# Kernel optimization log

Hardware: AMD Instinct MI355X
Metric: run time of the kernel (lower is better)

The kernel has to match this reference:

```python
import jax, jax.numpy as jnp
import numpy as np

N = 50000          # number of parent nodes / neighborhoods
D_IN = 256         # input_size
K = 8              # points decoded per neighborhood
GLOBAL_DIMS = [256, 128, 64]
FC_DIMS = [256, 256, 256]


def _linear_params(key, d_in, d_out):
    kw, kb = jax.random.split(key)
    W = jax.random.normal(kw, (d_in, d_out), dtype=jnp.float32) * 0.05
    b = jax.random.normal(kb, (d_out,), dtype=jnp.float32) * 0.05
    return W, b


def setup_inputs() -> dict:
    key = jax.random.key(0)
    keys = jax.random.split(key, 8)
    inp = {"input_features": jax.random.normal(keys[0], (N, D_IN), dtype=jnp.float32)}
    # global MLP: 256 -> 256 -> 128 -> 64
    d = D_IN
    for i, nb in enumerate(GLOBAL_DIMS):
        W, b = _linear_params(keys[1 + i], d, nb)
        inp[f"Wg{i}"], inp[f"bg{i}"] = W, b
        d = nb
    # neighborhood decoder head: 64 -> K*3
    inp["Wdec"], inp["bdec"] = _linear_params(keys[4], GLOBAL_DIMS[-1], K * 3)
    # per-point MLP: (256 + 64 + 3) -> 256 -> 256 -> 256
    d = D_IN + GLOBAL_DIMS[-1] + 3
    for i, nb in enumerate(FC_DIMS):
        W, b = _linear_params(keys[5 + i], d, nb)
        inp[f"W{i}"], inp[f"b{i}"] = W, b
        d = nb
    return inp


def reference(input_features, Wg0, bg0, Wg1, bg1, Wg2, bg2, Wdec, bdec,
              W0, b0, W1, b1, W2, b2):
    relu = jax.nn.relu
    # global feature MLP on node features: [N, 256] -> [N, 64]
    feats = input_features
    for W, b in ((Wg0, bg0), (Wg1, bg1), (Wg2, bg2)):
        feats = relu(feats @ W + b)
    # neighborhood decoder: K relative 3D points per node -> [N*K, 3]
    relative_points = (feats @ Wdec + bdec).reshape(-1, 3)
    cluster = jnp.repeat(jnp.arange(N, dtype=jnp.int32), K)  # [N*K]
    # gather (duplicate) parent features per decoded point
    nbr_dup = jnp.take(feats, cluster, axis=0)               # [N*K, 64]
    inp_dup = jnp.take(input_features, cluster, axis=0)      # [N*K, 256]
    decoded = jnp.concatenate([inp_dup, nbr_dup, relative_points], axis=1)  # [N*K, 323]
    for W, b in ((W0, b0), (W1, b1), (W2, b2)):
        decoded = relu(decoded @ W + b)
    return relative_points, decoded, cluster
```

## Files before the change

kernel.cpp:

```cpp
#include <hip/hip_runtime.h>
#include <hip/hip_bf16.h>

typedef __attribute__((ext_vector_type(8))) __bf16 bf16x8;
typedef __attribute__((ext_vector_type(4))) float f32x4;

#define NN 50000
#define TM1 16
#define NODES2 8


__device__ __forceinline__ unsigned short f2bf(float f) {
    unsigned int u = __builtin_bit_cast(unsigned int, f);
    u = (u + 0x7FFFu + ((u >> 16) & 1u)) >> 16;
    return (unsigned short)u;
}

__global__ __launch_bounds__(256) void k_prep(
    const float* __restrict__ W0, const float* __restrict__ W1,
    const float* __restrict__ W2, unsigned short* __restrict__ wbf)
{
    int idx = blockIdx.x * 256 + threadIdx.x;
    if (idx < 81920) {
        int n = idx / 320, k = idx - n * 320;
        wbf[idx] = f2bf(W0[(size_t)k * 256 + n]);
    } else if (idx < 147456) {
        int e = idx - 81920;
        int n = e >> 8, k = e & 255;
        wbf[idx] = f2bf(W1[(size_t)k * 256 + n]);
    } else if (idx < 212992) {
        int e = idx - 147456;
        int n = e >> 8, k = e & 255;
        wbf[idx] = f2bf(W2[(size_t)k * 256 + n]);
    }
}

__global__ __launch_bounds__(256) void k_global(
    const float* __restrict__ x,
    const float* __restrict__ Wg0, const float* __restrict__ bg0,
    const float* __restrict__ Wg1, const float* __restrict__ bg1,
    const float* __restrict__ Wg2, const float* __restrict__ bg2,
    const float* __restrict__ Wdec, const float* __restrict__ bdec,
    float* __restrict__ feats_ws,
    float* __restrict__ out_rel,
    float* __restrict__ out_cluster)
{
    __shared__ __attribute__((aligned(16))) float xin[TM1 * 256];
    __shared__ __attribute__((aligned(16))) float h0[TM1 * 256];
    __shared__ __attribute__((aligned(16))) float g1[TM1 * 128];
    __shared__ __attribute__((aligned(16))) float g2[TM1 * 64];

    const int tid = threadIdx.x;
    const int blk = blockIdx.x;

    {
        const float4* xg = (const float4*)(x + (size_t)blk * TM1 * 256);
        float4* xl = (float4*)xin;
        #pragma unroll
        for (int it = 0; it < 4; ++it) xl[tid + it * 256] = xg[tid + it * 256];
    }
    __syncthreads();

    {
        const int j = tid;
        float acc[TM1];
        float b = bg0[j];
        #pragma unroll
        for (int m = 0; m < TM1; ++m) acc[m] = b;
        for (int i = 0; i < 256; i += 4) {
            float w0 = Wg0[(size_t)(i + 0) * 256 + j];
            float w1 = Wg0[(size_t)(i + 1) * 256 + j];
            float w2 = Wg0[(size_t)(i + 2) * 256 + j];
            float w3 = Wg0[(size_t)(i + 3) * 256 + j];
            #pragma unroll
            for (int m = 0; m < TM1; ++m) {
                float4 xv = *(const float4*)&xin[m * 256 + i];
                acc[m] += xv.x * w0 + xv.y * w1 + xv.z * w2 + xv.w * w3;
            }
        }
        #pragma unroll
        for (int m = 0; m < TM1; ++m) h0[m * 256 + j] = fmaxf(acc[m], 0.f);
    }
    __syncthreads();

    {
        const int col = tid & 127;
        const int rg  = tid >> 7;
        float acc[8];
        float b = bg1[col];
        #pragma unroll
        for (int m = 0; m < 8; ++m) acc[m] = b;
        for (int i = 0; i < 256; i += 4) {
            float w0 = Wg1[(size_t)(i + 0) * 128 + col];
            float w1 = Wg1[(size_t)(i + 1) * 128 + col];
            float w2 = Wg1[(size_t)(i + 2) * 128 + col];
            float w3 = Wg1[(size_t)(i + 3) * 128 + col];
            #pragma unroll
            for (int m = 0; m < 8; ++m) {
                int r = rg * 8 + m;
                float4 xv = *(const float4*)&h0[r * 256 + i];
                acc[m] += xv.x * w0 + xv.y * w1 + xv.z * w2 + xv.w * w3;
            }
        }
        #pragma unroll
        for (int m = 0; m < 8; ++m) g1[(rg * 8 + m) * 128 + col] = fmaxf(acc[m], 0.f);
    }
    __syncthreads();

    {
        const int col = tid & 63;
        const int rg  = tid >> 6;
        float acc[4];
        float b = bg2[col];
        #pragma unroll
        for (int m = 0; m < 4; ++m) acc[m] = b;
        for (int i = 0; i < 128; i += 4) {
            float w0 = Wg2[(size_t)(i + 0) * 64 + col];
            float w1 = Wg2[(size_t)(i + 1) * 64 + col];
            float w2 = Wg2[(size_t)(i + 2) * 64 + col];
            float w3 = Wg2[(size_t)(i + 3) * 64 + col];
            #pragma unroll
            for (int m = 0; m < 4; ++m) {
                int r = rg * 4 + m;
                float4 xv = *(const float4*)&g1[r * 128 + i];
                acc[m] += xv.x * w0 + xv.y * w1 + xv.z * w2 + xv.w * w3;
            }
        }
        #pragma unroll
        for (int m = 0; m < 4; ++m) g2[(rg * 4 + m) * 64 + col] = fmaxf(acc[m], 0.f);
    }
    __syncthreads();

    {
        float4* fw = (float4*)(feats_ws + (size_t)blk * TM1 * 64);
        fw[tid] = ((const float4*)g2)[tid];
    }

    for (int tt = tid; tt < TM1 * 24; tt += 256) {
        int m = tt / 24;
        int c = tt - m * 24;
        float acc = bdec[c];
        for (int i = 0; i < 64; ++i) acc += g2[m * 64 + i] * Wdec[i * 24 + c];
        out_rel[(size_t)blk * (TM1 * 24) + tt] = acc;
    }

    if (tid < TM1 * 8) {
        out_cluster[(size_t)blk * (TM1 * 8) + tid] = (float)(blk * TM1 + (tid >> 3));
    }
}

__global__ __launch_bounds__(256) void k_points(
    const float* __restrict__ x,
    const float* __restrict__ feats_ws,
    const float* __restrict__ rel_in,
    const unsigned short* __restrict__ wbf,
    const float* __restrict__ W0f,
    const float* __restrict__ b0,
    const float* __restrict__ b1,
    const float* __restrict__ b2,
    float* __restrict__ out_dec)
{
    __shared__ __attribute__((aligned(16))) unsigned short h0s[64 * 264];
    __shared__ __attribute__((aligned(16))) unsigned short h1s[64 * 264];
    __shared__ __attribute__((aligned(16))) unsigned short xcat[NODES2 * 336];
    __shared__ __attribute__((aligned(16))) float w3buf[3 * 256];
    __shared__ __attribute__((aligned(16))) float rl[NODES2 * 24];
    float* s = (float*)h1s;

    const int tid  = threadIdx.x;
    const int lane = tid & 63;
    const int w    = tid >> 6;
    const int quad = lane >> 4;
    const int l15  = lane & 15;
    const int blk  = blockIdx.x;
    const size_t nb = (size_t)blk * NODES2;

    for (int e = tid; e < NODES2 * 256; e += 256) {
        int r = e >> 8, c = e & 255;
        xcat[r * 336 + c] = f2bf(x[(nb + r) * 256 + c]);
    }
    for (int e = tid; e < NODES2 * 64; e += 256) {
        int r = e >> 6, c = e & 63;
        xcat[r * 336 + 256 + c] = f2bf(feats_ws[(nb + r) * 64 + c]);
    }
    for (int e = tid; e < 3 * 256; e += 256) {
        int r = e >> 8, c = e & 255;
        w3buf[e] = W0f[(size_t)(320 + r) * 256 + c];
    }
    if (tid < NODES2 * 24) rl[tid] = rel_in[nb * 24 + tid];
    __syncthreads();

    {
        const unsigned short* W0t = wbf;
        f32x4 acc[4];
        f32x4 z = {0.f, 0.f, 0.f, 0.f};
        #pragma unroll
        for (int t = 0; t < 4; ++t) acc[t] = z;
        const unsigned short* arow = &xcat[(lane & 7) * 336];
        for (int ks = 0; ks < 10; ++ks) {
            int k0 = ks * 32 + quad * 8;
            bf16x8 a = *(const bf16x8*)(arow + k0);
            #pragma unroll
            for (int t = 0; t < 4; ++t) {
                int n = w * 64 + t * 16 + l15;
                bf16x8 b = *(const bf16x8*)(W0t + (size_t)n * 320 + k0);
                acc[t] = __builtin_amdgcn_mfma_f32_16x16x32_bf16(a, b, acc[t], 0, 0, 0);
            }
        }
        #pragma unroll
        for (int t = 0; t < 4; ++t) {
            int col = w * 64 + t * 16 + l15;
            float bb = b0[col];
            #pragma unroll
            for (int r = 0; r < 4; ++r) {
                int row = quad * 4 + r;
                if (row < NODES2) s[row * 256 + col] = acc[t][r] + bb;
            }
        }
    }
    __syncthreads();

    for (int it = 0; it < 16; ++it) {
        int task = tid + it * 256;
        int row = task >> 6;
        int cg  = task & 63;
        int node = row >> 3, p = row & 7;
        float4 sv = *(const float4*)&s[node * 256 + cg * 4];
        float ra = rl[node * 24 + p * 3 + 0];
        float rb = rl[node * 24 + p * 3 + 1];
        float rc = rl[node * 24 + p * 3 + 2];
        float4 wa = *(const float4*)&w3buf[cg * 4];
        float4 wbv = *(const float4*)&w3buf[256 + cg * 4];
        float4 wc = *(const float4*)&w3buf[512 + cg * 4];
        float v0 = fmaxf(sv.x + ra * wa.x + rb * wbv.x + rc * wc.x, 0.f);
        float v1 = fmaxf(sv.y + ra * wa.y + rb * wbv.y + rc * wc.y, 0.f);
        float v2 = fmaxf(sv.z + ra * wa.z + rb * wbv.z + rc * wc.z, 0.f);
        float v3 = fmaxf(sv.w + ra * wa.w + rb * wbv.w + rc * wc.w, 0.f);
        unsigned int lo = (unsigned int)f2bf(v0) | ((unsigned int)f2bf(v1) << 16);
        unsigned int hi = (unsigned int)f2bf(v2) | ((unsigned int)f2bf(v3) << 16);
        uint2 pk; pk.x = lo; pk.y = hi;
        *(uint2*)&h0s[row * 264 + cg * 4] = pk;
    }
    __syncthreads();

    {
        const unsigned short* W1t = wbf + 81920;
        f32x4 acc[4][4];
        f32x4 z = {0.f, 0.f, 0.f, 0.f};
        #pragma unroll
        for (int m = 0; m < 4; ++m)
            #pragma unroll
            for (int t = 0; t < 4; ++t) acc[m][t] = z;
        for (int ks = 0; ks < 8; ++ks) {
            int k0 = ks * 32 + quad * 8;
            bf16x8 a[4], b[4];
            #pragma unroll
            for (int m = 0; m < 4; ++m)
                a[m] = *(const bf16x8*)&h0s[(m * 16 + l15) * 264 + k0];
            #pragma unroll
            for (int t = 0; t < 4; ++t)
                b[t] = *(const bf16x8*)(W1t + (size_t)(w * 64 + t * 16 + l15) * 256 + k0);
            #pragma unroll
            for (int m = 0; m < 4; ++m)
                #pragma unroll
                for (int t = 0; t < 4; ++t)
                    acc[m][t] = __builtin_amdgcn_mfma_f32_16x16x32_bf16(a[m], b[t], acc[m][t], 0, 0, 0);
        }
        #pragma unroll
        for (int t = 0; t < 4; ++t) {
            int col = w * 64 + t * 16 + l15;
            float bb = b1[col];
            #pragma unroll
            for (int m = 0; m < 4; ++m) {
                #pragma unroll
                for (int r = 0; r < 4; ++r) {
                    int row = m * 16 + quad * 4 + r;
                    h1s[row * 264 + col] = f2bf(fmaxf(acc[m][t][r] + bb, 0.f));
                }
            }
        }
    }
    __syncthreads();

    {
        const unsigned short* W2t = wbf + 147456;
        f32x4 acc[4][4];
        f32x4 z = {0.f, 0.f, 0.f, 0.f};
        #pragma unroll
        for (int m = 0; m < 4; ++m)
            #pragma unroll
            for (int t = 0; t < 4; ++t) acc[m][t] = z;
        for (int ks = 0; ks < 8; ++ks) {
            int k0 = ks * 32 + quad * 8;
            bf16x8 a[4], b[4];
            #pragma unroll
            for (int m = 0; m < 4; ++m)
                a[m] = *(const bf16x8*)&h1s[(m * 16 + l15) * 264 + k0];
            #pragma unroll
            for (int t = 0; t < 4; ++t)
                b[t] = *(const bf16x8*)(W2t + (size_t)(w * 64 + t * 16 + l15) * 256 + k0);
            #pragma unroll
            for (int m = 0; m < 4; ++m)
                #pragma unroll
                for (int t = 0; t < 4; ++t)
                    acc[m][t] = __builtin_amdgcn_mfma_f32_16x16x32_bf16(a[m], b[t], acc[m][t], 0, 0, 0);
        }
        #pragma unroll
        for (int t = 0; t < 4; ++t) {
            int col = w * 64 + t * 16 + l15;
            float bb = b2[col];
            #pragma unroll
            for (int m = 0; m < 4; ++m) {
                #pragma unroll
                for (int r = 0; r < 4; ++r) {
                    int row = m * 16 + quad * 4 + r;
                    out_dec[(nb * 8 + row) * 256 + col] = fmaxf(acc[m][t][r] + bb, 0.f);
                }
            }
        }
    }
}

extern "C" void kernel_launch(void* const* d_in, const int* in_sizes, int n_in,
                              void* d_out, int out_size, void* d_ws, size_t ws_size,
                              hipStream_t stream) {
    const float* x    = (const float*)d_in[0];
    const float* Wg0  = (const float*)d_in[1];
    const float* bg0  = (const float*)d_in[2];
    const float* Wg1  = (const float*)d_in[3];
    const float* bg1  = (const float*)d_in[4];
    const float* Wg2  = (const float*)d_in[5];
    const float* bg2  = (const float*)d_in[6];
    const float* Wdec = (const float*)d_in[7];
    const float* bdec = (const float*)d_in[8];
    const float* W0   = (const float*)d_in[9];
    const float* b0   = (const float*)d_in[10];
    const float* W1   = (const float*)d_in[11];
    const float* b1   = (const float*)d_in[12];
    const float* W2   = (const float*)d_in[13];
    const float* b2   = (const float*)d_in[14];

    float* out      = (float*)d_out;
    float* out_rel  = out;
    float* out_dec  = out + 1200000;
    float* out_clu  = out + 103600000;

    unsigned short* wbf = (unsigned short*)d_ws;
    float* feats_ws = (float*)((char*)d_ws + 425984);

    k_prep<<<832, 256, 0, stream>>>(W0, W1, W2, wbf);
    k_global<<<NN / TM1, 256, 0, stream>>>(x, Wg0, bg0, Wg1, bg1, Wg2, bg2,
                                           Wdec, bdec, feats_ws, out_rel, out_clu);
    k_points<<<NN / NODES2, 256, 0, stream>>>(x, feats_ws, out_rel,
                                              wbf, W0, b0, b1, b2, out_dec);
}
```

Measured before the change: 1.059 ms.

## Run global MLP on MFMA with split-bf16 hi/lo emulation of fp32

The global 3-layer MLP moves from scalar fp32 FMA loops onto bf16 MFMA instructions. Activations and weights are split into high and low bf16 parts, using three MFMAs per step to keep close to fp32 accuracy. Weight transposition and splitting are added to the prep kernel. Node features are now stored as bf16, which halves that traffic and lets k_points copy them directly without converting. The costs are three times the MFMA work, extra LDS buffers, and a small precision change in the stored features.

```diff
diff --git a/kernel.cpp b/kernel.cpp
--- a/kernel.cpp
+++ b/kernel.cpp
@@ -3,21 +3,31 @@
 
 typedef __attribute__((ext_vector_type(8))) __bf16 bf16x8;
 typedef __attribute__((ext_vector_type(4))) float f32x4;
+typedef __attribute__((ext_vector_type(4))) unsigned short u16x4;
 
 #define NN 50000
 #define TM1 16
 #define NODES2 8
 
+
+#define FEATS_OFF 212992
+#define GW_OFF    3412992
 
 __device__ __forceinline__ unsigned short f2bf(float f) {
     unsigned int u = __builtin_bit_cast(unsigned int, f);
     u = (u + 0x7FFFu + ((u >> 16) & 1u)) >> 16;
     return (unsigned short)u;
 }
+__device__ __forceinline__ float bf2f(unsigned short h) {
+    return __builtin_bit_cast(float, (unsigned int)h << 16);
+}
 
 __global__ __launch_bounds__(256) void k_prep(
     const float* __restrict__ W0, const float* __restrict__ W1,
-    const float* __restrict__ W2, unsigned short* __restrict__ wbf)
+    const float* __restrict__ W2,
+    const float* __restrict__ Wg0, const float* __restrict__ Wg1,
+    const float* __restrict__ Wg2,
+    unsigned short* __restrict__ wbf)
 {
     int idx = blockIdx.x * 256 + threadIdx.x;
     if (idx < 81920) {
@@ -31,108 +41,168 @@
         int e = idx - 147456;
         int n = e >> 8, k = e & 255;
         wbf[idx] = f2bf(W2[(size_t)k * 256 + n]);
+    } else if (idx < 319488) {
+        int e = idx - 212992;
+        float v; int oh, ol;
+        if (e < 65536) {
+            int n = e >> 8, k = e & 255;
+            v = Wg0[(size_t)k * 256 + n];
+            oh = GW_OFF + e; ol = GW_OFF + 65536 + e;
+        } else if (e < 98304) {
+            int e2 = e - 65536;
+            int n = e2 >> 8, k = e2 & 255;
+            v = Wg1[(size_t)k * 128 + n];
+            oh = GW_OFF + 131072 + e2; ol = GW_OFF + 163840 + e2;
+        } else {
+            int e3 = e - 98304;
+            int n = e3 >> 7, k = e3 & 127;
+            v = Wg2[(size_t)k * 64 + n];
+            oh = GW_OFF + 196608 + e3; ol = GW_OFF + 204800 + e3;
+        }
+        unsigned short h = f2bf(v);
+        wbf[oh] = h;
+        wbf[ol] = f2bf(v - bf2f(h));
     }
 }
 
 __global__ __launch_bounds__(256) void k_global(
     const float* __restrict__ x,
-    const float* __restrict__ Wg0, const float* __restrict__ bg0,
-    const float* __restrict__ Wg1, const float* __restrict__ bg1,
-    const float* __restrict__ Wg2, const float* __restrict__ bg2,
+    const float* __restrict__ bg0, const float* __restrict__ bg1,
+    const float* __restrict__ bg2,
     const float* __restrict__ Wdec, const float* __restrict__ bdec,
-    float* __restrict__ feats_ws,
+    const unsigned short* __restrict__ gw,
+    unsigned short* __restrict__ feats_bf,
     float* __restrict__ out_rel,
     float* __restrict__ out_cluster)
 {
-    __shared__ __attribute__((aligned(16))) float xin[TM1 * 256];
-    __shared__ __attribute__((aligned(16))) float h0[TM1 * 256];
-    __shared__ __attribute__((aligned(16))) float g1[TM1 * 128];
+    __shared__ __attribute__((aligned(16))) unsigned short xh[TM1 * 264];
+    __shared__ __attribute__((aligned(16))) unsigned short xl[TM1 * 264];
+    __shared__ __attribute__((aligned(16))) unsigned short hh[TM1 * 264];
+    __shared__ __attribute__((aligned(16))) unsigned short hl[TM1 * 264];
+    __shared__ __attribute__((aligned(16))) unsigned short q1h[TM1 * 136];
+    __shared__ __attribute__((aligned(16))) unsigned short q1l[TM1 * 136];
     __shared__ __attribute__((aligned(16))) float g2[TM1 * 64];
 
-    const int tid = threadIdx.x;
-    const int blk = blockIdx.x;
-
-    {
-        const float4* xg = (const float4*)(x + (size_t)blk * TM1 * 256);
-        float4* xl = (float4*)xin;
-        #pragma unroll
-        for (int it = 0; it < 4; ++it) xl[tid + it * 256] = xg[tid + it * 256];
-    }
-    __syncthreads();
-
-    {
-        const int j = tid;
-        float acc[TM1];
-        float b = bg0[j];
-        #pragma unroll
-        for (int m = 0; m < TM1; ++m) acc[m] = b;
-        for (int i = 0; i < 256; i += 4) {
-            float w0 = Wg0[(size_t)(i + 0) * 256 + j];
-            float w1 = Wg0[(size_t)(i + 1) * 256 + j];
-            float w2 = Wg0[(size_t)(i + 2) * 256 + j];
-            float w3 = Wg0[(size_t)(i + 3) * 256 + j];
-            #pragma unroll
-            for (int m = 0; m < TM1; ++m) {
-                float4 xv = *(const float4*)&xin[m * 256 + i];
-                acc[m] += xv.x * w0 + xv.y * w1 + xv.z * w2 + xv.w * w3;
-            }
-        }
-        #pragma unroll
-        for (int m = 0; m < TM1; ++m) h0[m * 256 + j] = fmaxf(acc[m], 0.f);
-    }
-    __syncthreads();
-
-    {
-        const int col = tid & 127;
-        const int rg  = tid >> 7;
-        float acc[8];
-        float b = bg1[col];
-        #pragma unroll
-        for (int m = 0; m < 8; ++m) acc[m] = b;
-        for (int i = 0; i < 256; i += 4) {
-            float w0 = Wg1[(size_t)(i + 0) * 128 + col];
-            float w1 = Wg1[(size_t)(i + 1) * 128 + col];
-            float w2 = Wg1[(size_t)(i + 2) * 128 + col];
-            float w3 = Wg1[(size_t)(i + 3) * 128 + col];
-            #pragma unroll
-            for (int m = 0; m < 8; ++m) {
-                int r = rg * 8 + m;
-                float4 xv = *(const float4*)&h0[r * 256 + i];
-                acc[m] += xv.x * w0 + xv.y * w1 + xv.z * w2 + xv.w * w3;
-            }
-        }
-        #pragma unroll
-        for (int m = 0; m < 8; ++m) g1[(rg * 8 + m) * 128 + col] = fmaxf(acc[m], 0.f);
-    }
-    __syncthreads();
-
-    {
-        const int col = tid & 63;
-        const int rg  = tid >> 6;
-        float acc[4];
-        float b = bg2[col];
-        #pragma unroll
-        for (int m = 0; m < 4; ++m) acc[m] = b;
-        for (int i = 0; i < 128; i += 4) {
-            float w0 = Wg2[(size_t)(i + 0) * 64 + col];
-            float w1 = Wg2[(size_t)(i + 1) * 64 + col];
-            float w2 = Wg2[(size_t)(i + 2) * 64 + col];
-            float w3 = Wg2[(size_t)(i + 3) * 64 + col];
-            #pragma unroll
-            for (int m = 0; m < 4; ++m) {
-                int r = rg * 4 + m;
-                float4 xv = *(const float4*)&g1[r * 128 + i];
-                acc[m] += xv.x * w0 + xv.y * w1 + xv.z * w2 + xv.w * w3;
-            }
-        }
-        #pragma unroll
-        for (int m = 0; m < 4; ++m) g2[(rg * 4 + m) * 64 + col] = fmaxf(acc[m], 0.f);
-    }
-    __syncthreads();
-
-    {
-        float4* fw = (float4*)(feats_ws + (size_t)blk * TM1 * 64);
-        fw[tid] = ((const float4*)g2)[tid];
+    const int tid  = threadIdx.x;
+    const int lane = tid & 63;
+    const int w    = tid >> 6;
+    const int quad = lane >> 4;
+    const int l15  = lane & 15;
+    const int blk  = blockIdx.x;
+
+    for (int e = tid; e < TM1 * 256; e += 256) {
+        int r = e >> 8, c = e & 255;
+        float v = x[(size_t)(blk * TM1 + r) * 256 + c];
+        unsigned short h = f2bf(v);
+        xh[r * 264 + c] = h;
+        xl[r * 264 + c] = f2bf(v - bf2f(h));
+    }
+    __syncthreads();
+
+    {
+        const unsigned short* Wh = gw;
+        const unsigned short* Wl = gw + 65536;
+        f32x4 acc[4];
+        f32x4 z = {0.f, 0.f, 0.f, 0.f};
+        #pragma unroll
+        for (int t = 0; t < 4; ++t) acc[t] = z;
+        for (int ks = 0; ks < 8; ++ks) {
+            int k0 = ks * 32 + quad * 8;
+            bf16x8 ah = *(const bf16x8*)&xh[l15 * 264 + k0];
+            bf16x8 al = *(const bf16x8*)&xl[l15 * 264 + k0];
+            #pragma unroll
+            for (int t = 0; t < 4; ++t) {
+                int n = w * 64 + t * 16 + l15;
+                bf16x8 bh = *(const bf16x8*)(Wh + (size_t)n * 256 + k0);
+                bf16x8 bl = *(const bf16x8*)(Wl + (size_t)n * 256 + k0);
+                acc[t] = __builtin_amdgcn_mfma_f32_16x16x32_bf16(ah, bh, acc[t], 0, 0, 0);
+                acc[t] = __builtin_amdgcn_mfma_f32_16x16x32_bf16(al, bh, acc[t], 0, 0, 0);
+                acc[t] = __builtin_amdgcn_mfma_f32_16x16x32_bf16(ah, bl, acc[t], 0, 0, 0);
+            }
+        }
+        #pragma unroll
+        for (int t = 0; t < 4; ++t) {
+            int col = w * 64 + t * 16 + l15;
+            float bb = bg0[col];
+            #pragma unroll
+            for (int r = 0; r < 4; ++r) {
+                int row = quad * 4 + r;
+                float v = fmaxf(acc[t][r] + bb, 0.f);
+                unsigned short h = f2bf(v);
+                hh[row * 264 + col] = h;
+                hl[row * 264 + col] = f2bf(v - bf2f(h));
+            }
+        }
+    }
+    __syncthreads();
+
+    {
+        const unsigned short* Wh = gw + 131072;
+        const unsigned short* Wl = gw + 163840;
+        f32x4 acc[2];
+        f32x4 z = {0.f, 0.f, 0.f, 0.f};
+        acc[0] = z; acc[1] = z;
+        for (int ks = 0; ks < 8; ++ks) {
+            int k0 = ks * 32 + quad * 8;
+            bf16x8 ah = *(const bf16x8*)&hh[l15 * 264 + k0];
+            bf16x8 al = *(const bf16x8*)&hl[l15 * 264 + k0];
+            #pragma unroll
+            for (int t = 0; t < 2; ++t) {
+                int n = w * 32 + t * 16 + l15;
+                bf16x8 bh = *(const bf16x8*)(Wh + (size_t)n * 256 + k0);
+                bf16x8 bl = *(const bf16x8*)(Wl + (size_t)n * 256 + k0);
+                acc[t] = __builtin_amdgcn_mfma_f32_16x16x32_bf16(ah, bh, acc[t], 0, 0, 0);
+                acc[t] = __builtin_amdgcn_mfma_f32_16x16x32_bf16(al, bh, acc[t], 0, 0, 0);
+                acc[t] = __builtin_amdgcn_mfma_f32_16x16x32_bf16(ah, bl, acc[t], 0, 0, 0);
+            }
+        }
+        #pragma unroll
+        for (int t = 0; t < 2; ++t) {
+            int col = w * 32 + t * 16 + l15;
+            float bb = bg1[col];
+            #pragma unroll
+            for (int r = 0; r < 4; ++r) {
+                int row = quad * 4 + r;
+                float v = fmaxf(acc[t][r] + bb, 0.f);
+                unsigned short h = f2bf(v);
+                q1h[row * 136 + col] = h;
+                q1l[row * 136 + col] = f2bf(v - bf2f(h));
+            }
+        }
+    }
+    __syncthreads();
+
+    {
+        const unsigned short* Wh = gw + 196608;
+        const unsigned short* Wl = gw + 204800;
+        f32x4 acc = {0.f, 0.f, 0.f, 0.f};
+        for (int ks = 0; ks < 4; ++ks) {
+            int k0 = ks * 32 + quad * 8;
+            bf16x8 ah = *(const bf16x8*)&q1h[l15 * 136 + k0];
+            bf16x8 al = *(const bf16x8*)&q1l[l15 * 136 + k0];
+            int n = w * 16 + l15;
+            bf16x8 bh = *(const bf16x8*)(Wh + (size_t)n * 128 + k0);
+            bf16x8 bl = *(const bf16x8*)(Wl + (size_t)n * 128 + k0);
+            acc = __builtin_amdgcn_mfma_f32_16x16x32_bf16(ah, bh, acc, 0, 0, 0);
+            acc = __builtin_amdgcn_mfma_f32_16x16x32_bf16(al, bh, acc, 0, 0, 0);
+            acc = __builtin_amdgcn_mfma_f32_16x16x32_bf16(ah, bl, acc, 0, 0, 0);
+        }
+        int col = w * 16 + l15;
+        float bb = bg2[col];
+        #pragma unroll
+        for (int r = 0; r < 4; ++r) {
+            int row = quad * 4 + r;
+            g2[row * 64 + col] = fmaxf(acc[r] + bb, 0.f);
+        }
+    }
+    __syncthreads();
+
+    {
+        const float* src = g2 + tid * 4;
+        u16x4 p;
+        p[0] = f2bf(src[0]); p[1] = f2bf(src[1]);
+        p[2] = f2bf(src[2]); p[3] = f2bf(src[3]);
+        *(u16x4*)&feats_bf[(size_t)blk * (TM1 * 64) + tid * 4] = p;
     }
 
     for (int tt = tid; tt < TM1 * 24; tt += 256) {
@@ -150,7 +220,7 @@
 
 __global__ __launch_bounds__(256) void k_points(
     const float* __restrict__ x,
-    const float* __restrict__ feats_ws,
+    const unsigned short* __restrict__ feats_bf,
     const float* __restrict__ rel_in,
     const unsigned short* __restrict__ wbf,
     const float* __restrict__ W0f,
@@ -178,9 +248,11 @@
         int r = e >> 8, c = e & 255;
         xcat[r * 336 + c] = f2bf(x[(nb + r) * 256 + c]);
     }
-    for (int e = tid; e < NODES2 * 64; e += 256) {
+    {
+        int e = tid * 2;
         int r = e >> 6, c = e & 63;
-        xcat[r * 336 + 256 + c] = f2bf(feats_ws[(nb + r) * 64 + c]);
+        *(unsigned int*)&xcat[r * 336 + 256 + c] =
+            *(const unsigned int*)&feats_bf[nb * 64 + e];
     }
     for (int e = tid; e < 3 * 256; e += 256) {
         int r = e >> 8, c = e & 255;
@@ -344,12 +416,13 @@
     float* out_dec  = out + 1200000;
     float* out_clu  = out + 103600000;
 
-    unsigned short* wbf = (unsigned short*)d_ws;
-    float* feats_ws = (float*)((char*)d_ws + 425984);
-
-    k_prep<<<832, 256, 0, stream>>>(W0, W1, W2, wbf);
-    k_global<<<NN / TM1, 256, 0, stream>>>(x, Wg0, bg0, Wg1, bg1, Wg2, bg2,
-                                           Wdec, bdec, feats_ws, out_rel, out_clu);
-    k_points<<<NN / NODES2, 256, 0, stream>>>(x, feats_ws, out_rel,
+    unsigned short* wbf      = (unsigned short*)d_ws;
+    unsigned short* feats_bf = wbf + FEATS_OFF;
+    unsigned short* gw       = wbf + GW_OFF;
+
+    k_prep<<<1248, 256, 0, stream>>>(W0, W1, W2, Wg0, Wg1, Wg2, wbf);
+    k_global<<<NN / TM1, 256, 0, stream>>>(x, bg0, bg1, bg2, Wdec, bdec, gw,
+                                           feats_bf, out_rel, out_clu);
+    k_points<<<NN / NODES2, 256, 0, stream>>>(x, feats_bf, out_rel,
                                               wbf, W0, b0, b1, b2, out_dec);
 }
```

Measured after the change: 979.2 us. 7.5% less time.
